# Kernel optimization log

Measured on AMD Instinct MI355X. Metric: run time of the kernel, lower is better.

## Reference

```python
import jax, jax.numpy as jnp
import numpy as np
from jax import lax

# ---- config (matches DecodePredictions init kwargs) ----
MAX_PER_CLASS = 100
MAX_TOTAL = 100
IOU_THRESH = 0.5
SCORE_THRESH = 0.05
NUM_CLASSES = 80
K_CAND = 512  # per-class candidate pool kept before NMS (bounds the O(K^2) IoU work)
BOX_VARIANCE = np.array([0.1, 0.1, 0.2, 0.2], np.float32)


def generate_anchors(height, width):
    """RetinaNet anchors (keras.io AnchorBox): FPN levels 3-7, 3 ratios x 3 scales, [cx,cy,w,h] in pixels."""
    ratios = [0.5, 1.0, 2.0]
    scales = [2 ** 0.0, 2 ** (1.0 / 3.0), 2 ** (2.0 / 3.0)]
    all_anchors = []
    for level in range(3, 8):
        stride = 2 ** level
        area = float((2 ** (level + 2)) ** 2)  # 32^2 .. 512^2
        dims = []
        for r in ratios:
            ah = np.sqrt(area / r)
            aw = area / ah
            for s in scales:
                dims.append([s * aw, s * ah])
        dims = np.asarray(dims, np.float32)  # [9, 2] = (w, h)
        fh = int(np.ceil(height / stride))
        fw = int(np.ceil(width / stride))
        rx = (np.arange(fw, dtype=np.float32) + 0.5) * stride
        ry = (np.arange(fh, dtype=np.float32) + 0.5) * stride
        cx, cy = np.meshgrid(rx, ry)
        centers = np.stack([cx, cy], -1)[:, :, None, :].repeat(9, axis=2)  # [fh,fw,9,2]
        d = np.broadcast_to(dims, (fh, fw, 9, 2))
        all_anchors.append(np.concatenate([centers, d], -1).reshape(-1, 4).astype(np.float32))
    return jnp.asarray(np.concatenate(all_anchors, 0))  # [N, 4]


def _pairwise_iou(b):
    # Generic TF NMS IoU formula treating coords as [y1,x1,y2,x2] (module feeds cx,cy,w,h -- replicated faithfully).
    y1, x1, y2, x2 = b[:, 0], b[:, 1], b[:, 2], b[:, 3]
    area = jnp.maximum(y2 - y1, 0.0) * jnp.maximum(x2 - x1, 0.0)
    ih = jnp.maximum(jnp.minimum(y2[:, None], y2[None, :]) - jnp.maximum(y1[:, None], y1[None, :]), 0.0)
    iw = jnp.maximum(jnp.minimum(x2[:, None], x2[None, :]) - jnp.maximum(x1[:, None], x1[None, :]), 0.0)
    inter = ih * iw
    union = area[:, None] + area[None, :] - inter
    return jnp.where(union > 0.0, inter / union, 0.0)


def _nms_single_class(boxes, scores):  # boxes [N,4], scores [N]
    top_s, idx = lax.top_k(scores, K_CAND)          # sort-by-score candidate pool
    top_b = boxes[idx]                               # [K,4]
    keep0 = top_s > SCORE_THRESH                     # score_threshold filter
    iou = _pairwise_iou(top_b)                       # [K,K]
    rng = jnp.arange(K_CAND)

    def body(i, keep):
        sup = (iou[i] > IOU_THRESH) & (rng > i)      # boxes ranked below i suppressed by i
        return jnp.where(keep[i], keep & ~sup, keep)

    keep = lax.fori_loop(0, K_CAND, body, keep0)
    kept_s = jnp.where(keep, top_s, 0.0)
    sel_s, sel = lax.top_k(kept_s, MAX_PER_CLASS)    # max_output_size_per_class
    return top_b[sel], sel_s                         # [P,4], [P]


def _combine(cls_boxes, cls_scores):  # [C,P,4], [C,P] -> combined top MAX_TOTAL for one image
    C, P = cls_scores.shape
    flat_s = cls_scores.reshape(-1)
    flat_b = cls_boxes.reshape(-1, 4)
    flat_c = jnp.repeat(jnp.arange(C, dtype=jnp.float32), P)
    top_s, idx = lax.top_k(flat_s, MAX_TOTAL)
    valid = (top_s > 0.0)
    vf = valid.astype(flat_b.dtype)
    boxes = jnp.clip(flat_b[idx], 0.0, 1.0) * vf[:, None]  # clip_boxes=True, zero-pad invalid
    scores = top_s * vf
    classes = jnp.where(valid, flat_c[idx], 0.0)
    return boxes, scores, classes, valid.sum().astype(jnp.int32)


def _forward(inputs, predictions):
    H, W = inputs.shape[1], inputs.shape[2]
    anchors = generate_anchors(float(H), float(W))            # [N,4] cx,cy,w,h
    cls_scores = jax.nn.sigmoid(predictions[..., :-4])        # [B,N,C]
    box_pred = predictions[..., -4:] * jnp.asarray(BOX_VARIANCE)
    xy = box_pred[..., :2] * anchors[..., 2:] + anchors[..., :2]
    wh = jnp.exp(box_pred[..., 2:]) * anchors[..., 2:]
    boxes = jnp.concatenate([xy, wh], -1)                     # [B,N,4] decoded

    per_class = jax.vmap(jax.vmap(_nms_single_class, in_axes=(None, 1)), in_axes=(0, 0))
    cb, cs = per_class(boxes, cls_scores)                     # [B,C,P,4], [B,C,P]
    return jax.vmap(_combine)(cb, cs)                         # boxes, scores, classes, valid


def setup_inputs() -> dict:
    key = jax.random.key(0)
    k1, k2 = jax.random.split(key)
    inputs = jax.random.uniform(k1, (4, 640, 640, 3), jnp.float32)
    predictions = jax.random.normal(k2, (4, 76725, NUM_CLASSES + 4), jnp.float32)
    return {"inputs": inputs, "predictions": predictions}


def reference(inputs, predictions):
    return _forward(inputs, predictions)
```

## Files before the change

kernel.cpp:

```cpp
#include <hip/hip_runtime.h>
#include <cmath>

#define NA 76725
#define NCLS 80
#define NB 4
#define KC 512
#define MPC 100
#define MT 100
#define TT 128
#define NTILE 600
#define NSLOTP 600
#define PADN 76800
#define CAP 4096
#define SLOT 16
#define SPLIT 8
#define THRESH_LOGIT 2.0f

struct Dims { float d[5 * 9 * 2]; };


__device__ __forceinline__ unsigned keyof(float x) {
    unsigned u = __float_as_uint(x);
    return u ^ ((u & 0x80000000u) ? 0xFFFFFFFFu : 0x80000000u);
}
__device__ __forceinline__ float unkey(unsigned k) {
    unsigned u = (k & 0x80000000u) ? (k ^ 0x80000000u) : ~k;
    return __uint_as_float(u);
}
__device__ __forceinline__ float sigmoidf_dev(float x) {
    if (x >= 0.f) return 1.f / (1.f + expf(-x));
    float e = expf(x);
    return e / (1.f + e);
}
__device__ __forceinline__ unsigned long long compose(unsigned key, int a) {
    return ((unsigned long long)key << 32) | (unsigned long long)(0xFFFFFFFFu - (unsigned)a);
}

__device__ __forceinline__ float4 decode_box(float4 p, int a, const Dims& dims) {
    const int base[5] = {0, 57600, 72000, 75600, 76500};
    const int fw[5] = {80, 40, 20, 10, 5};
    const float strd[5] = {8.f, 16.f, 32.f, 64.f, 128.f};
    int l;
    if (a < 57600) l = 0;
    else if (a < 72000) l = 1;
    else if (a < 75600) l = 2;
    else if (a < 76500) l = 3;
    else l = 4;
    int i = a - base[l];
    int cell = i / 9, k = i - cell * 9;
    int x = cell % fw[l], y = cell / fw[l];
    float cx = ((float)x + 0.5f) * strd[l];
    float cy = ((float)y + 0.5f) * strd[l];
    float aw = dims.d[(l * 9 + k) * 2 + 0];
    float ah = dims.d[(l * 9 + k) * 2 + 1];
    float bx = __fmul_rn(p.x, 0.1f), by = __fmul_rn(p.y, 0.1f);
    float bw = __fmul_rn(p.z, 0.2f), bh = __fmul_rn(p.w, 0.2f);
    float4 o;
    o.x = __fadd_rn(__fmul_rn(bx, aw), cx);
    o.y = __fadd_rn(__fmul_rn(by, ah), cy);
    o.z = __fmul_rn(expf(bw), aw);
    o.w = __fmul_rn(expf(bh), ah);
    return o;
}


__global__ __launch_bounds__(256) void scan_kernel(const float* __restrict__ pred,
                                                   unsigned long long* __restrict__ candbuf,
                                                   int* __restrict__ counts2) {
    __shared__ int cnt[NCLS];
    const int blk = blockIdx.x;
    const int b = blk / NTILE, tix = blk - b * NTILE;
    const int t0 = tix * TT;
    int nrow = NA - t0; if (nrow > TT) nrow = TT;

    if (threadIdx.x < NCLS) cnt[threadIdx.x] = 0;
    __syncthreads();

    const float4* src = reinterpret_cast<const float4*>(pred + ((size_t)b * NA + t0) * 84);
    const int nv = nrow * 21;
    unsigned long long* slotbase = candbuf + (size_t)(b * NCLS) * NSLOTP * SLOT + (size_t)tix * SLOT;
    for (int i = threadIdx.x; i < nv; i += 256) {
        const float4 v = src[i];
        const int row = i / 21, chunk = i - row * 21;
        if (chunk == 20) continue;
        const int a = t0 + row, cbase = chunk * 4;
        const float vals[4] = {v.x, v.y, v.z, v.w};
        #pragma unroll
        for (int q = 0; q < 4; ++q) {
            if (vals[q] > THRESH_LOGIT) {
                const int c = cbase + q;
                const int p = atomicAdd(&cnt[c], 1);
                if (p < SLOT)
                    slotbase[(size_t)c * NSLOTP * SLOT + p] = compose(keyof(vals[q]), a);
            }
        }
    }
    __syncthreads();
    if (threadIdx.x < NCLS)
        counts2[(size_t)(b * NCLS + threadIdx.x) * NSLOTP + tix] = cnt[threadIdx.x];
}


__device__ __forceinline__ void find_bin(int* hist, int bins, int remaining,
                                         int* sh3, int* wsum) {
    const int tid = threadIdx.x;
    const int lane = tid & 63, wv = tid >> 6;
    const int nit = (bins + 1023) >> 10;
    int lsum = 0;
    for (int q = 0; q < nit; ++q) {
        int rr = tid * nit + q;
        if (rr < bins) lsum += hist[bins - 1 - rr];
    }
    int acc = lsum;
    #pragma unroll
    for (int off = 1; off < 64; off <<= 1) {
        int x = __shfl_up(acc, off);
        if (lane >= off) acc += x;
    }
    if (lane == 63) wsum[wv] = acc;
    __syncthreads();
    int base = 0;
    for (int w = 0; w < wv; ++w) base += wsum[w];
    int run = base + acc - lsum;
    for (int q = 0; q < nit; ++q) {
        int rr = tid * nit + q;
        if (rr < bins) {
            int h = hist[bins - 1 - rr];
            if (run < remaining && remaining <= run + h) { sh3[0] = bins - 1 - rr; sh3[1] = run; sh3[2] = h; }
            run += h;
        }
    }
    __syncthreads();
}


__global__ __launch_bounds__(1024) void topk2_kernel(const float* __restrict__ pred,
                                                     const unsigned long long* __restrict__ candbuf,
                                                     const int* __restrict__ counts2,
                                                     float* __restrict__ top_score,
                                                     float4* __restrict__ sel_boxes, Dims dims) {
    const int col = blockIdx.x;
    const int b = col / NCLS, cc = col - b * NCLS;
    const int tid = threadIdx.x;
    const int lane = tid & 63, wv = tid >> 6;

    __shared__ unsigned long long cand[CAP];
    __shared__ int hist[256];
    __shared__ unsigned long long buf[KC];
    __shared__ int scnt[NSLOTP];
    __shared__ int spfx[NSLOTP];
    __shared__ int sh3[3];
    __shared__ int wsum[16];
    __shared__ int gcount, eqtaken, totsh, ovfsh;
    __shared__ int wcnt[16];
    int* hist4k = (int*)cand;

    if (tid == 0) { totsh = 0; ovfsh = 0; }
    if (tid < NSLOTP) scnt[tid] = counts2[(size_t)col * NSLOTP + tid];
    __syncthreads();

    int lsum = (tid < NSLOTP) ? scnt[tid] : 0;
    if (lsum > SLOT) ovfsh = 1;
    int acc = lsum;
    #pragma unroll
    for (int off = 1; off < 64; off <<= 1) {
        int x = __shfl_up(acc, off);
        if (lane >= off) acc += x;
    }
    if (lane == 63) wsum[wv] = acc;
    __syncthreads();
    int base = 0;
    for (int w = 0; w < wv; ++w) base += wsum[w];
    if (tid < NSLOTP) spfx[tid] = base + acc - lsum;
    if (tid == 1023) totsh = base + acc;
    __syncthreads();

    const int tot = totsh;
    const bool fastok = (!ovfsh) && tot >= KC && tot <= CAP;
    int nc = -1;

    if (fastok) {
        const unsigned long long* src = candbuf + (size_t)col * NSLOTP * SLOT;
        for (int i = tid; i < NSLOTP * SLOT; i += 1024) {
            const int e = i >> 4, q = i & (SLOT - 1);
            const unsigned long long v = src[i];
            if (q < scnt[e]) cand[spfx[e] + q] = v;
        }
        nc = tot;
        __syncthreads();
    } else {
        const float* colp = pred + (size_t)b * NA * 84 + cc;
        for (int i = tid; i < 4096; i += 1024) hist4k[i] = 0;
        __syncthreads();
        for (int a = tid; a < NA; a += 1024)
            atomicAdd(&hist4k[keyof(colp[(size_t)a * 84]) >> 20], 1);
        __syncthreads();
        find_bin(hist4k, 4096, KC, sh3, wsum);
        const int bsel = sh3[0], above = sh3[1], ceq1 = sh3[2];
        const int ncand = above + ceq1;

        if (ncand <= CAP) {
            const unsigned fk = ((unsigned)bsel) << 20;
            if (tid == 0) gcount = 0;
            __syncthreads();
            for (int a = tid; a < NA; a += 1024) {
                unsigned k = keyof(colp[(size_t)a * 84]);
                if (k >= fk) { int p = atomicAdd(&gcount, 1); cand[p] = compose(k, a); }
            }
            __syncthreads();
            nc = gcount;
        } else {
            unsigned prefix = ((unsigned)bsel) << 20;
            int remaining = KC - above;

            for (int i = tid; i < 4096; i += 1024) hist4k[i] = 0;
            __syncthreads();
            for (int a = tid; a < NA; a += 1024) {
                unsigned k = keyof(colp[(size_t)a * 84]);
                if ((k & 0xFFF00000u) == prefix) atomicAdd(&hist4k[(k >> 8) & 4095], 1);
            }
            __syncthreads();
            find_bin(hist4k, 4096, remaining, sh3, wsum);
            prefix |= ((unsigned)sh3[0]) << 8;
            remaining -= sh3[1];

            if (tid < 256) hist[tid] = 0;
            __syncthreads();
            for (int a = tid; a < NA; a += 1024) {
                unsigned k = keyof(colp[(size_t)a * 84]);
                if ((k & 0xFFFFFF00u) == prefix) atomicAdd(&hist[k & 255], 1);
            }
            __syncthreads();
            find_bin(hist, 256, remaining, sh3, wsum);
            prefix |= (unsigned)sh3[0];
            remaining -= sh3[1];

            const unsigned K = prefix;
            const int cgt = KC - remaining;
            const int need = remaining;
            if (tid == 0) { gcount = 0; eqtaken = 0; }
            __syncthreads();
            for (int bs = 0; bs < PADN; bs += 1024) {
                int a = bs + tid;
                unsigned key = (a < NA) ? keyof(colp[(size_t)a * 84]) : 0u;
                if (a < NA && key > K) {
                    int p = atomicAdd(&gcount, 1);
                    buf[p] = compose(key, a);
                }
                bool eq = (key == K) && (a < NA);
                unsigned long long m = __ballot(eq);
                if (lane == 0) wcnt[wv] = __popcll(m);
                __syncthreads();
                int off = eqtaken;
                for (int w = 0; w < wv; ++w) off += wcnt[w];
                int rank = off + __popcll(m & ((1ull << lane) - 1ull));
                if (eq && rank < need)
                    buf[cgt + rank] = compose(K, a);
                __syncthreads();
                if (tid == 0) {
                    int s = 0;
                    for (int w = 0; w < 16; ++w) s += wcnt[w];
                    eqtaken += s;
                }
                __syncthreads();
            }
            nc = -1;
        }
    }

    if (nc >= 0) {
        unsigned long long cpre = 0ull;
        int rem512 = KC;
        for (int pass = 0; pass < 8; ++pass) {
            const int shift = 56 - 8 * pass;
            const unsigned long long mdone = pass ? ((~0ull) << (shift + 8)) : 0ull;
            if (tid < 256) hist[tid] = 0;
            __syncthreads();
            for (int t = tid; t < nc; t += 1024) {
                unsigned long long k = cand[t];
                if ((k & mdone) == cpre) atomicAdd(&hist[(int)((k >> shift) & 255)], 1);
            }
            __syncthreads();
            find_bin(hist, 256, rem512, sh3, wsum);
            cpre |= ((unsigned long long)(unsigned)sh3[0]) << shift;
            rem512 -= sh3[1];
            __syncthreads();
        }
        if (tid == 0) gcount = 0;
        __syncthreads();
        for (int t = tid; t < nc; t += 1024) {
            unsigned long long k = cand[t];
            if (k >= cpre) { int p = atomicAdd(&gcount, 1); buf[p] = k; }
        }
        __syncthreads();
    }

    for (int k2 = 2; k2 <= KC; k2 <<= 1) {
        for (int j = k2 >> 1; j > 0; j >>= 1) {
            __syncthreads();
            if (tid < KC) {
                int i = tid, ixj = i ^ j;
                if (ixj > i) {
                    unsigned long long A = buf[i], B = buf[ixj];
                    bool up = (i & k2) == 0;
                    if (up ? (A < B) : (A > B)) { buf[i] = B; buf[ixj] = A; }
                }
            }
        }
    }
    __syncthreads();
    if (tid < KC) {
        unsigned long long v = buf[tid];
        unsigned key = (unsigned)(v >> 32);
        int a = (int)(0xFFFFFFFFu - (unsigned)(v & 0xFFFFFFFFu));
        top_score[col * KC + tid] = sigmoidf_dev(unkey(key));
        const float4 p4 = *reinterpret_cast<const float4*>(pred + ((size_t)b * NA + a) * 84 + 80);
        sel_boxes[(size_t)col * KC + tid] = decode_box(p4, a, dims);
    }
}


__global__ __launch_bounds__(512) void nms_build_kernel(const float4* __restrict__ sel_boxes,
                                                        unsigned long long* __restrict__ maskbuf) {
    const int blk = blockIdx.x;
    const int col = blk >> 3, part = blk & 7;
    const int tid = threadIdx.x, wave = tid >> 6, lane = tid & 63;
    __shared__ float y1[KC], x1[KC], y2[KC], x2[KC], ar[KC];

    for (int t = tid; t < KC; t += 512) {
        float4 bx = sel_boxes[(size_t)col * KC + t];
        y1[t] = bx.x; x1[t] = bx.y; y2[t] = bx.z; x2[t] = bx.w;
        ar[t] = __fmul_rn(fmaxf(__fsub_rn(bx.z, bx.x), 0.f),
                          fmaxf(__fsub_rn(bx.w, bx.y), 0.f));
    }
    __syncthreads();

    float jy1[8], jx1[8], jy2[8], jx2[8], jar[8];
    #pragma unroll
    for (int w = 0; w < 8; ++w) {
        int j = (w << 6) + lane;
        jy1[w] = y1[j]; jx1[w] = x1[j]; jy2[w] = y2[j]; jx2[w] = x2[j]; jar[w] = ar[j];
    }

    for (int k = 0; k < 8; ++k) {
        const int i = part + SPLIT * (wave + 8 * k);
        const float iy1 = y1[i], ix1 = x1[i], iy2 = y2[i], ix2 = x2[i], iar = ar[i];
        unsigned long long row[8];
        #pragma unroll
        for (int w = 0; w < 8; ++w) {
            unsigned long long m = 0ull;
            if (((w << 6) + 63) > i) {
                const int j = (w << 6) + lane;
                float ih = fmaxf(__fsub_rn(fminf(iy2, jy2[w]), fmaxf(iy1, jy1[w])), 0.f);
                float iw = fmaxf(__fsub_rn(fminf(ix2, jx2[w]), fmaxf(ix1, jx1[w])), 0.f);
                float inter = __fmul_rn(ih, iw);
                float uni = __fsub_rn(__fadd_rn(iar, jar[w]), inter);
                m = __ballot((uni > 0.f) && (inter > __fmul_rn(0.5f, uni)) && (j > i));
            }
            row[w] = m;
        }
        unsigned long long v = row[0];
        v = (lane == 1) ? row[1] : v;
        v = (lane == 2) ? row[2] : v;
        v = (lane == 3) ? row[3] : v;
        v = (lane == 4) ? row[4] : v;
        v = (lane == 5) ? row[5] : v;
        v = (lane == 6) ? row[6] : v;
        v = (lane == 7) ? row[7] : v;
        if (lane < 8) maskbuf[((size_t)col * KC + i) * 8 + lane] = v;
    }
}


__global__ __launch_bounds__(256) void nms_resolve_kernel(const float4* __restrict__ sel_boxes,
                                                          const float* __restrict__ top_score,
                                                          const unsigned long long* __restrict__ maskbuf,
                                                          float4* __restrict__ col_boxes,
                                                          float* __restrict__ col_scores) {
    const int col = blockIdx.x;
    const int tid = threadIdx.x, wv = tid >> 6, lane = tid & 63;
    __shared__ unsigned long long mask[KC * 8];
    __shared__ float y1[KC], x1[KC], y2[KC], x2[KC], sc[KC];
    __shared__ unsigned long long keep0w[8], keepw[8];
    __shared__ int wordpfx[9];
    __shared__ int sel[MPC];

    {
        const unsigned long long* src = maskbuf + (size_t)col * KC * 8;
        for (int m = tid; m < KC * 8; m += 256) mask[m] = src[m];
    }
    for (int t = tid; t < KC; t += 256) {
        float4 bx = sel_boxes[(size_t)col * KC + t];
        y1[t] = bx.x; x1[t] = bx.y; y2[t] = bx.z; x2[t] = bx.w;
        const float s = top_score[col * KC + t];
        sc[t] = s;
        const unsigned long long m = __ballot(s > 0.05f);
        if (lane == 0) keep0w[t >> 6] = m;
    }
    __syncthreads();

    if (wv == 0) {
        const int w8 = lane & 7;
        const unsigned long long kww = keep0w[w8];
        unsigned long long remw = 0ull;
        for (int ib = 0; ib < KC; ib += 8) {
            unsigned long long rows[8];
            #pragma unroll
            for (int u = 0; u < 8; ++u) rows[u] = mask[(ib + u) * 8 + w8];
            #pragma unroll
            for (int u = 0; u < 8; ++u) {
                const int i = ib + u, W = i >> 6, t = i & 63;
                const unsigned long long remW = __shfl(remw, W);
                const unsigned long long kwW = __shfl(kww, W);
                if (((kwW >> t) & 1ull) && !((remW >> t) & 1ull)) remw |= rows[u];
            }
        }
        if (lane < 8) keepw[w8] = kww & ~remw;
    }
    __syncthreads();
    if (tid == 0) {
        int s = 0;
        #pragma unroll
        for (int w = 0; w < 8; ++w) { wordpfx[w] = s; s += __popcll(keepw[w]); }
        wordpfx[8] = s;
    }
    __syncthreads();

    const int nkept = wordpfx[8];
    for (int t = tid; t < KC; t += 256) {
        const unsigned long long w = keepw[t >> 6];
        const int l = t & 63;
        const bool kp = (w >> l) & 1ull;
        const int kb = wordpfx[t >> 6] + __popcll(w & ((1ull << l) - 1ull));
        if (kp) {
            if (kb < MPC) sel[kb] = t;
        } else {
            const int nb = t - kb;
            if (nkept + nb < MPC) sel[nkept + nb] = t;
        }
    }
    __syncthreads();
    if (tid < MPC) {
        int t = sel[tid];
        bool kp = (keepw[t >> 6] >> (t & 63)) & 1ull;
        col_scores[col * MPC + tid] = kp ? sc[t] : 0.f;
        col_boxes[col * MPC + tid] = make_float4(y1[t], x1[t], y2[t], x2[t]);
    }
}


__global__ __launch_bounds__(1024) void combine_kernel(const float4* __restrict__ col_boxes,
                                                       const float* __restrict__ col_scores,
                                                       float* __restrict__ out) {
    const int b = blockIdx.x, tid = threadIdx.x;
    const int wv = tid >> 6, lane = tid & 63;
    __shared__ int hist[256];
    __shared__ unsigned long long cand[128];
    __shared__ int sh3[3];
    __shared__ int gcnt, eqtaken;
    __shared__ int wcnt[16];
    __shared__ int wsc[16];

    const int NTOT = NCLS * MPC;
    unsigned sck[8];
    #pragma unroll
    for (int q = 0; q < 8; ++q) {
        const int t = (q << 10) + tid;
        sck[q] = (t < NTOT) ? __float_as_uint(col_scores[b * NTOT + t]) : 0u;
    }

    unsigned prefix = 0;
    int remaining = MT, ceq = 0;
    #pragma unroll 1
    for (int pass = 0; pass < 4; ++pass) {
        const int shift = 24 - 8 * pass;
        const unsigned mdone = pass ? (0xFFFFFFFFu << (shift + 8)) : 0u;
        if (tid < 256) hist[tid] = 0;
        __syncthreads();
        #pragma unroll
        for (int q = 0; q < 8; ++q) {
            const int t = (q << 10) + tid;
            if (t < NTOT && (sck[q] & mdone) == prefix)
                atomicAdd(&hist[(sck[q] >> shift) & 255], 1);
        }
        __syncthreads();
        int lsum = (tid < 256) ? hist[255 - tid] : 0;
        int acc2 = lsum;
        #pragma unroll
        for (int off = 1; off < 64; off <<= 1) {
            int x = __shfl_up(acc2, off);
            if (lane >= off) acc2 += x;
        }
        if (lane == 63) wsc[wv] = acc2;
        __syncthreads();
        int base2 = 0;
        for (int w = 0; w < wv; ++w) base2 += wsc[w];
        int run = base2 + acc2 - lsum;
        if (tid < 256 && run < remaining && remaining <= run + lsum) { sh3[0] = 255 - tid; sh3[1] = run; sh3[2] = lsum; }
        __syncthreads();
        prefix |= ((unsigned)sh3[0]) << shift;
        remaining -= sh3[1];
        ceq = sh3[2];
        __syncthreads();
    }
    const unsigned S = prefix;
    const int cgt = MT - remaining;

    if (tid == 0) { gcnt = 0; eqtaken = 0; }
    if (tid < 128) cand[tid] = 0ull;
    __syncthreads();
    #pragma unroll
    for (int q = 0; q < 8; ++q) {
        const int t = (q << 10) + tid;
        if (t < NTOT && sck[q] > S) {
            int p = atomicAdd(&gcnt, 1);
            cand[p] = ((unsigned long long)sck[q] << 32) |
                      (unsigned long long)(0xFFFFFFFFu - (unsigned)t);
        }
    }
    __syncthreads();

    if (ceq == remaining) {
        #pragma unroll
        for (int q = 0; q < 8; ++q) {
            const int t = (q << 10) + tid;
            if (t < NTOT && sck[q] == S) {
                int p = atomicAdd(&eqtaken, 1);
                cand[cgt + p] = ((unsigned long long)S << 32) |
                                (unsigned long long)(0xFFFFFFFFu - (unsigned)t);
            }
        }
        __syncthreads();
    } else {
        #pragma unroll 1
        for (int q = 0; q < 8; ++q) {
            const int t = (q << 10) + tid;
            const bool eq = (t < NTOT) && (sck[q] == S);
            unsigned long long m = __ballot(eq);
            if (lane == 0) wcnt[wv] = __popcll(m);
            __syncthreads();
            int off = eqtaken;
            for (int w = 0; w < wv; ++w) off += wcnt[w];
            int rank = off + __popcll(m & ((1ull << lane) - 1ull));
            if (eq && rank < remaining)
                cand[cgt + rank] = ((unsigned long long)S << 32) |
                                   (unsigned long long)(0xFFFFFFFFu - (unsigned)t);
            __syncthreads();
            if (tid == 0) {
                int s = 0;
                for (int w = 0; w < 16; ++w) s += wcnt[w];
                eqtaken += s;
            }
            __syncthreads();
        }
    }

    for (int k2 = 2; k2 <= 128; k2 <<= 1) {
        for (int j = k2 >> 1; j > 0; j >>= 1) {
            __syncthreads();
            if (tid < 128) {
                int i = tid, ixj = i ^ j;
                if (ixj > i) {
                    unsigned long long A = cand[i], B = cand[ixj];
                    bool up = (i & k2) == 0;
                    if (up ? (A < B) : (A > B)) { cand[i] = B; cand[ixj] = A; }
                }
            }
        }
    }
    __syncthreads();
    if (tid == 0) gcnt = 0;
    __syncthreads();
    if (tid < MT) {
        unsigned long long v = cand[tid];
        float s = __uint_as_float((unsigned)(v >> 32));
        int f = (int)(0xFFFFFFFFu - (unsigned)(v & 0xFFFFFFFFu));
        bool valid = (s > 0.f);
        int cl = 0, p = 0;
        float4 bx = make_float4(0.f, 0.f, 0.f, 0.f);
        if (valid) {
            cl = f / MPC;
            p = f - cl * MPC;
            float4 raw = col_boxes[((size_t)b * NCLS + cl) * MPC + p];
            bx.x = fminf(fmaxf(raw.x, 0.f), 1.f);
            bx.y = fminf(fmaxf(raw.y, 0.f), 1.f);
            bx.z = fminf(fmaxf(raw.z, 0.f), 1.f);
            bx.w = fminf(fmaxf(raw.w, 0.f), 1.f);
            atomicAdd(&gcnt, 1);
        }
        int o = b * MT + tid;
        out[o * 4 + 0] = bx.x;
        out[o * 4 + 1] = bx.y;
        out[o * 4 + 2] = bx.z;
        out[o * 4 + 3] = bx.w;
        out[NB * MT * 4 + o] = valid ? s : 0.f;
        out[NB * MT * 5 + o] = valid ? (float)cl : 0.f;
    }
    __syncthreads();
    if (tid == 0) out[NB * MT * 6 + b] = (float)gcnt;
}


extern "C" void kernel_launch(void* const* d_in, const int* in_sizes, int n_in,
                              void* d_out, int out_size, void* d_ws, size_t ws_size,
                              hipStream_t stream) {
    const float* pred = (const float*)d_in[1];
    float* out = (float*)d_out;
    char* ws = (char*)d_ws;

    Dims dims;
    const double ratios[3] = {0.5, 1.0, 2.0};
    for (int l = 0; l < 5; ++l) {
        double side = (double)(1 << (l + 5));
        double area = side * side;
        for (int ri = 0; ri < 3; ++ri) {
            double ah = sqrt(area / ratios[ri]);
            double aw = area / ah;
            for (int si = 0; si < 3; ++si) {
                double s = pow(2.0, (double)si / 3.0);
                dims.d[(l * 9 + ri * 3 + si) * 2 + 0] = (float)(s * aw);
                dims.d[(l * 9 + ri * 3 + si) * 2 + 1] = (float)(s * ah);
            }
        }
    }

    const size_t SZ_CAND = (size_t)NB * NCLS * NSLOTP * SLOT * 8;
    const size_t SZ_CNT  = (size_t)NB * NCLS * NSLOTP * 4;
    const size_t SZ_SC   = (size_t)NB * NCLS * KC * 4;
    const size_t SZ_SEL  = (size_t)NB * NCLS * KC * 16;
    const size_t SZ_CB   = (size_t)NB * NCLS * MPC * 16;

    unsigned long long* candbuf    = (unsigned long long*)(ws);
    int*                counts2    = (int*)(ws + SZ_CAND);
    float*              top_score  = (float*)(ws + SZ_CAND + SZ_CNT);
    float4*             sel_boxes  = (float4*)(ws + SZ_CAND + SZ_CNT + SZ_SC);
    float4*             col_boxes  = (float4*)(ws + SZ_CAND + SZ_CNT + SZ_SC + SZ_SEL);
    float*              col_scores = (float*)(ws + SZ_CAND + SZ_CNT + SZ_SC + SZ_SEL + SZ_CB);
    unsigned long long* maskbuf    = (unsigned long long*)(ws);

    scan_kernel<<<NB * NTILE, 256, 0, stream>>>(pred, candbuf, counts2);
    topk2_kernel<<<NB * NCLS, 1024, 0, stream>>>(pred, candbuf, counts2, top_score, sel_boxes, dims);
    nms_build_kernel<<<NB * NCLS * SPLIT, 512, 0, stream>>>(sel_boxes, maskbuf);
    nms_resolve_kernel<<<NB * NCLS, 256, 0, stream>>>(sel_boxes, top_score, maskbuf, col_boxes, col_scores);
    combine_kernel<<<NB, 1024, 0, stream>>>(col_boxes, col_scores, out);
}
```

Before: 321.8 us.

## Fuse top-k selection, NMS mask build and resolve into one kernel

Merges the top-k, NMS mask-build and NMS resolve kernels into a single 512-thread per-column kernel. Boxes, scores and the suppression mask now stay in shared memory instead of going through global buffers, which removes two launches and the intermediate traffic. The scan kernel's candidate buffer changes to a tile-major layout so each tile writes contiguously, and its loop is unrolled four times to issue more loads in flight. The cost is less parallelism in mask building: 320 blocks each compute all 512 rows instead of 2560 blocks, so per-block work rises.

```diff
diff --git a/kernel.cpp b/kernel.cpp
--- a/kernel.cpp
+++ b/kernel.cpp
@@ -10,10 +10,10 @@
 #define TT 128
 #define NTILE 600
 #define NSLOTP 600
+#define NSLOTPAD 1024
 #define PADN 76800
 #define CAP 4096
 #define SLOT 16
-#define SPLIT 8
 #define THRESH_LOGIT 2.0f
 
 struct Dims { float d[5 * 9 * 2]; };
@@ -78,23 +78,39 @@
 
     const float4* src = reinterpret_cast<const float4*>(pred + ((size_t)b * NA + t0) * 84);
     const int nv = nrow * 21;
-    unsigned long long* slotbase = candbuf + (size_t)(b * NCLS) * NSLOTP * SLOT + (size_t)tix * SLOT;
-    for (int i = threadIdx.x; i < nv; i += 256) {
+    unsigned long long* slotbase = candbuf + (size_t)(b * NTILE + tix) * NCLS * SLOT;
+
+    #define PROC(v, idx) do {                                                  \
+        const int row_ = (idx) / 21, chunk_ = (idx) - row_ * 21;               \
+        if (chunk_ != 20) {                                                    \
+            const int a_ = t0 + row_, cbase_ = chunk_ * 4;                     \
+            const float vals_[4] = {(v).x, (v).y, (v).z, (v).w};               \
+            _Pragma("unroll")                                                  \
+            for (int q_ = 0; q_ < 4; ++q_) {                                   \
+                if (vals_[q_] > THRESH_LOGIT) {                                \
+                    const int c_ = cbase_ + q_;                                \
+                    const int p_ = atomicAdd(&cnt[c_], 1);                     \
+                    if (p_ < SLOT)                                             \
+                        slotbase[c_ * SLOT + p_] = compose(keyof(vals_[q_]), a_); \
+                }                                                              \
+            }                                                                  \
+        }                                                                      \
+    } while (0)
+
+    int i = threadIdx.x;
+    for (; i + 768 < nv; i += 1024) {
+        const float4 v0 = src[i];
+        const float4 v1 = src[i + 256];
+        const float4 v2 = src[i + 512];
+        const float4 v3 = src[i + 768];
+        PROC(v0, i); PROC(v1, i + 256); PROC(v2, i + 512); PROC(v3, i + 768);
+    }
+    for (; i < nv; i += 256) {
         const float4 v = src[i];
-        const int row = i / 21, chunk = i - row * 21;
-        if (chunk == 20) continue;
-        const int a = t0 + row, cbase = chunk * 4;
-        const float vals[4] = {v.x, v.y, v.z, v.w};
-        #pragma unroll
-        for (int q = 0; q < 4; ++q) {
-            if (vals[q] > THRESH_LOGIT) {
-                const int c = cbase + q;
-                const int p = atomicAdd(&cnt[c], 1);
-                if (p < SLOT)
-                    slotbase[(size_t)c * NSLOTP * SLOT + p] = compose(keyof(vals[q]), a);
-            }
-        }
-    }
+        PROC(v, i);
+    }
+    #undef PROC
+
     __syncthreads();
     if (threadIdx.x < NCLS)
         counts2[(size_t)(b * NCLS + threadIdx.x) * NSLOTP + tix] = cnt[threadIdx.x];
@@ -105,7 +121,7 @@
                                          int* sh3, int* wsum) {
     const int tid = threadIdx.x;
     const int lane = tid & 63, wv = tid >> 6;
-    const int nit = (bins + 1023) >> 10;
+    const int nit = (bins + 511) >> 9;
     int lsum = 0;
     for (int q = 0; q < nit; ++q) {
         int rr = tid * nit + q;
@@ -134,11 +150,11 @@
 }
 
 
-__global__ __launch_bounds__(1024) void topk2_kernel(const float* __restrict__ pred,
+__global__ __launch_bounds__(512) void topnms_kernel(const float* __restrict__ pred,
                                                      const unsigned long long* __restrict__ candbuf,
                                                      const int* __restrict__ counts2,
-                                                     float* __restrict__ top_score,
-                                                     float4* __restrict__ sel_boxes, Dims dims) {
+                                                     float4* __restrict__ col_boxes,
+                                                     float* __restrict__ col_scores, Dims dims) {
     const int col = blockIdx.x;
     const int b = col / NCLS, cc = col - b * NCLS;
     const int tid = threadIdx.x;
@@ -147,21 +163,28 @@
     __shared__ unsigned long long cand[CAP];
     __shared__ int hist[256];
     __shared__ unsigned long long buf[KC];
-    __shared__ int scnt[NSLOTP];
-    __shared__ int spfx[NSLOTP];
+    __shared__ int scnt[NSLOTPAD];
+    __shared__ int spfx[NSLOTPAD];
+    __shared__ float y1[KC], x1[KC], y2[KC], x2[KC], ar[KC], sc[KC];
+    __shared__ unsigned long long keep0w[8], keepw[8];
+    __shared__ int wordpfx[9];
+    __shared__ int sel[MPC];
     __shared__ int sh3[3];
-    __shared__ int wsum[16];
+    __shared__ int wsum[8];
     __shared__ int gcount, eqtaken, totsh, ovfsh;
-    __shared__ int wcnt[16];
+    __shared__ int wcnt[8];
     int* hist4k = (int*)cand;
+    unsigned long long* maskl = cand;
 
     if (tid == 0) { totsh = 0; ovfsh = 0; }
-    if (tid < NSLOTP) scnt[tid] = counts2[(size_t)col * NSLOTP + tid];
-    __syncthreads();
-
-    int lsum = (tid < NSLOTP) ? scnt[tid] : 0;
-    if (lsum > SLOT) ovfsh = 1;
-    int acc = lsum;
+    for (int i = tid; i < NSLOTPAD; i += 512)
+        scnt[i] = (i < NSLOTP) ? counts2[(size_t)col * NSLOTP + i] : 0;
+    __syncthreads();
+
+    const int c0s = scnt[2 * tid], c1s = scnt[2 * tid + 1];
+    if (c0s > SLOT || c1s > SLOT) ovfsh = 1;
+    const int pair = c0s + c1s;
+    int acc = pair;
     #pragma unroll
     for (int off = 1; off < 64; off <<= 1) {
         int x = __shfl_up(acc, off);
@@ -171,8 +194,10 @@
     __syncthreads();
     int base = 0;
     for (int w = 0; w < wv; ++w) base += wsum[w];
-    if (tid < NSLOTP) spfx[tid] = base + acc - lsum;
-    if (tid == 1023) totsh = base + acc;
+    const int excl = base + acc - pair;
+    spfx[2 * tid] = excl;
+    spfx[2 * tid + 1] = excl + c0s;
+    if (tid == 511) totsh = base + acc;
     __syncthreads();
 
     const int tot = totsh;
@@ -180,19 +205,19 @@
     int nc = -1;
 
     if (fastok) {
-        const unsigned long long* src = candbuf + (size_t)col * NSLOTP * SLOT;
-        for (int i = tid; i < NSLOTP * SLOT; i += 1024) {
+        const size_t colbase = (size_t)(b * NTILE) * (NCLS * SLOT) + (size_t)cc * SLOT;
+        for (int i = tid; i < NSLOTP * SLOT; i += 512) {
             const int e = i >> 4, q = i & (SLOT - 1);
-            const unsigned long long v = src[i];
+            const unsigned long long v = candbuf[colbase + (size_t)e * (NCLS * SLOT) + q];
             if (q < scnt[e]) cand[spfx[e] + q] = v;
         }
         nc = tot;
         __syncthreads();
     } else {
         const float* colp = pred + (size_t)b * NA * 84 + cc;
-        for (int i = tid; i < 4096; i += 1024) hist4k[i] = 0;
-        __syncthreads();
-        for (int a = tid; a < NA; a += 1024)
+        for (int i = tid; i < 4096; i += 512) hist4k[i] = 0;
+        __syncthreads();
+        for (int a = tid; a < NA; a += 512)
             atomicAdd(&hist4k[keyof(colp[(size_t)a * 84]) >> 20], 1);
         __syncthreads();
         find_bin(hist4k, 4096, KC, sh3, wsum);
@@ -203,7 +228,7 @@
             const unsigned fk = ((unsigned)bsel) << 20;
             if (tid == 0) gcount = 0;
             __syncthreads();
-            for (int a = tid; a < NA; a += 1024) {
+            for (int a = tid; a < NA; a += 512) {
                 unsigned k = keyof(colp[(size_t)a * 84]);
                 if (k >= fk) { int p = atomicAdd(&gcount, 1); cand[p] = compose(k, a); }
             }
@@ -213,9 +238,9 @@
             unsigned prefix = ((unsigned)bsel) << 20;
             int remaining = KC - above;
 
-            for (int i = tid; i < 4096; i += 1024) hist4k[i] = 0;
-            __syncthreads();
-            for (int a = tid; a < NA; a += 1024) {
+            for (int i = tid; i < 4096; i += 512) hist4k[i] = 0;
+            __syncthreads();
+            for (int a = tid; a < NA; a += 512) {
                 unsigned k = keyof(colp[(size_t)a * 84]);
                 if ((k & 0xFFF00000u) == prefix) atomicAdd(&hist4k[(k >> 8) & 4095], 1);
             }
@@ -226,7 +251,7 @@
 
             if (tid < 256) hist[tid] = 0;
             __syncthreads();
-            for (int a = tid; a < NA; a += 1024) {
+            for (int a = tid; a < NA; a += 512) {
                 unsigned k = keyof(colp[(size_t)a * 84]);
                 if ((k & 0xFFFFFF00u) == prefix) atomicAdd(&hist[k & 255], 1);
             }
@@ -240,7 +265,7 @@
             const int need = remaining;
             if (tid == 0) { gcount = 0; eqtaken = 0; }
             __syncthreads();
-            for (int bs = 0; bs < PADN; bs += 1024) {
+            for (int bs = 0; bs < PADN; bs += 512) {
                 int a = bs + tid;
                 unsigned key = (a < NA) ? keyof(colp[(size_t)a * 84]) : 0u;
                 if (a < NA && key > K) {
@@ -259,7 +284,7 @@
                 __syncthreads();
                 if (tid == 0) {
                     int s = 0;
-                    for (int w = 0; w < 16; ++w) s += wcnt[w];
+                    for (int w = 0; w < 8; ++w) s += wcnt[w];
                     eqtaken += s;
                 }
                 __syncthreads();
@@ -276,7 +301,7 @@
             const unsigned long long mdone = pass ? ((~0ull) << (shift + 8)) : 0ull;
             if (tid < 256) hist[tid] = 0;
             __syncthreads();
-            for (int t = tid; t < nc; t += 1024) {
+            for (int t = tid; t < nc; t += 512) {
                 unsigned long long k = cand[t];
                 if ((k & mdone) == cpre) atomicAdd(&hist[(int)((k >> shift) & 255)], 1);
             }
@@ -288,7 +313,7 @@
         }
         if (tid == 0) gcount = 0;
         __syncthreads();
-        for (int t = tid; t < nc; t += 1024) {
+        for (int t = tid; t < nc; t += 512) {
             unsigned long long k = cand[t];
             if (k >= cpre) { int p = atomicAdd(&gcount, 1); buf[p] = k; }
         }
@@ -298,7 +323,7 @@
     for (int k2 = 2; k2 <= KC; k2 <<= 1) {
         for (int j = k2 >> 1; j > 0; j >>= 1) {
             __syncthreads();
-            if (tid < KC) {
+            {
                 int i = tid, ixj = i ^ j;
                 if (ixj > i) {
                     unsigned long long A = buf[i], B = buf[ixj];
@@ -309,93 +334,57 @@
         }
     }
     __syncthreads();
-    if (tid < KC) {
-        unsigned long long v = buf[tid];
-        unsigned key = (unsigned)(v >> 32);
-        int a = (int)(0xFFFFFFFFu - (unsigned)(v & 0xFFFFFFFFu));
-        top_score[col * KC + tid] = sigmoidf_dev(unkey(key));
+
+    {
+        const unsigned long long v = buf[tid];
+        const unsigned key = (unsigned)(v >> 32);
+        const int a = (int)(0xFFFFFFFFu - (unsigned)(v & 0xFFFFFFFFu));
+        const float s = sigmoidf_dev(unkey(key));
+        sc[tid] = s;
         const float4 p4 = *reinterpret_cast<const float4*>(pred + ((size_t)b * NA + a) * 84 + 80);
-        sel_boxes[(size_t)col * KC + tid] = decode_box(p4, a, dims);
-    }
-}
-
-
-__global__ __launch_bounds__(512) void nms_build_kernel(const float4* __restrict__ sel_boxes,
-                                                        unsigned long long* __restrict__ maskbuf) {
-    const int blk = blockIdx.x;
-    const int col = blk >> 3, part = blk & 7;
-    const int tid = threadIdx.x, wave = tid >> 6, lane = tid & 63;
-    __shared__ float y1[KC], x1[KC], y2[KC], x2[KC], ar[KC];
-
-    for (int t = tid; t < KC; t += 512) {
-        float4 bx = sel_boxes[(size_t)col * KC + t];
-        y1[t] = bx.x; x1[t] = bx.y; y2[t] = bx.z; x2[t] = bx.w;
-        ar[t] = __fmul_rn(fmaxf(__fsub_rn(bx.z, bx.x), 0.f),
-                          fmaxf(__fsub_rn(bx.w, bx.y), 0.f));
-    }
-    __syncthreads();
-
-    float jy1[8], jx1[8], jy2[8], jx2[8], jar[8];
-    #pragma unroll
-    for (int w = 0; w < 8; ++w) {
-        int j = (w << 6) + lane;
-        jy1[w] = y1[j]; jx1[w] = x1[j]; jy2[w] = y2[j]; jx2[w] = x2[j]; jar[w] = ar[j];
-    }
-
-    for (int k = 0; k < 8; ++k) {
-        const int i = part + SPLIT * (wave + 8 * k);
-        const float iy1 = y1[i], ix1 = x1[i], iy2 = y2[i], ix2 = x2[i], iar = ar[i];
-        unsigned long long row[8];
+        const float4 bx = decode_box(p4, a, dims);
+        y1[tid] = bx.x; x1[tid] = bx.y; y2[tid] = bx.z; x2[tid] = bx.w;
+        ar[tid] = __fmul_rn(fmaxf(__fsub_rn(bx.z, bx.x), 0.f),
+                            fmaxf(__fsub_rn(bx.w, bx.y), 0.f));
+        const unsigned long long m = __ballot(s > 0.05f);
+        if (lane == 0) keep0w[tid >> 6] = m;
+    }
+    __syncthreads();
+
+    {
+        float jy1[8], jx1[8], jy2[8], jx2[8], jar[8];
         #pragma unroll
         for (int w = 0; w < 8; ++w) {
-            unsigned long long m = 0ull;
-            if (((w << 6) + 63) > i) {
-                const int j = (w << 6) + lane;
-                float ih = fmaxf(__fsub_rn(fminf(iy2, jy2[w]), fmaxf(iy1, jy1[w])), 0.f);
-                float iw = fmaxf(__fsub_rn(fminf(ix2, jx2[w]), fmaxf(ix1, jx1[w])), 0.f);
-                float inter = __fmul_rn(ih, iw);
-                float uni = __fsub_rn(__fadd_rn(iar, jar[w]), inter);
-                m = __ballot((uni > 0.f) && (inter > __fmul_rn(0.5f, uni)) && (j > i));
-            }
-            row[w] = m;
-        }
-        unsigned long long v = row[0];
-        v = (lane == 1) ? row[1] : v;
-        v = (lane == 2) ? row[2] : v;
-        v = (lane == 3) ? row[3] : v;
-        v = (lane == 4) ? row[4] : v;
-        v = (lane == 5) ? row[5] : v;
-        v = (lane == 6) ? row[6] : v;
-        v = (lane == 7) ? row[7] : v;
-        if (lane < 8) maskbuf[((size_t)col * KC + i) * 8 + lane] = v;
-    }
-}
-
-
-__global__ __launch_bounds__(256) void nms_resolve_kernel(const float4* __restrict__ sel_boxes,
-                                                          const float* __restrict__ top_score,
-                                                          const unsigned long long* __restrict__ maskbuf,
-                                                          float4* __restrict__ col_boxes,
-                                                          float* __restrict__ col_scores) {
-    const int col = blockIdx.x;
-    const int tid = threadIdx.x, wv = tid >> 6, lane = tid & 63;
-    __shared__ unsigned long long mask[KC * 8];
-    __shared__ float y1[KC], x1[KC], y2[KC], x2[KC], sc[KC];
-    __shared__ unsigned long long keep0w[8], keepw[8];
-    __shared__ int wordpfx[9];
-    __shared__ int sel[MPC];
-
-    {
-        const unsigned long long* src = maskbuf + (size_t)col * KC * 8;
-        for (int m = tid; m < KC * 8; m += 256) mask[m] = src[m];
-    }
-    for (int t = tid; t < KC; t += 256) {
-        float4 bx = sel_boxes[(size_t)col * KC + t];
-        y1[t] = bx.x; x1[t] = bx.y; y2[t] = bx.z; x2[t] = bx.w;
-        const float s = top_score[col * KC + t];
-        sc[t] = s;
-        const unsigned long long m = __ballot(s > 0.05f);
-        if (lane == 0) keep0w[t >> 6] = m;
+            int j = (w << 6) + lane;
+            jy1[w] = y1[j]; jx1[w] = x1[j]; jy2[w] = y2[j]; jx2[w] = x2[j]; jar[w] = ar[j];
+        }
+        for (int k = 0; k < 64; ++k) {
+            const int i = wv + 8 * k;
+            const float iy1 = y1[i], ix1 = x1[i], iy2 = y2[i], ix2 = x2[i], iar = ar[i];
+            unsigned long long row[8];
+            #pragma unroll
+            for (int w = 0; w < 8; ++w) {
+                unsigned long long m = 0ull;
+                if (((w << 6) + 63) > i) {
+                    const int j = (w << 6) + lane;
+                    float ih = fmaxf(__fsub_rn(fminf(iy2, jy2[w]), fmaxf(iy1, jy1[w])), 0.f);
+                    float iw = fmaxf(__fsub_rn(fminf(ix2, jx2[w]), fmaxf(ix1, jx1[w])), 0.f);
+                    float inter = __fmul_rn(ih, iw);
+                    float uni = __fsub_rn(__fadd_rn(iar, jar[w]), inter);
+                    m = __ballot((uni > 0.f) && (inter > __fmul_rn(0.5f, uni)) && (j > i));
+                }
+                row[w] = m;
+            }
+            unsigned long long v = row[0];
+            v = (lane == 1) ? row[1] : v;
+            v = (lane == 2) ? row[2] : v;
+            v = (lane == 3) ? row[3] : v;
+            v = (lane == 4) ? row[4] : v;
+            v = (lane == 5) ? row[5] : v;
+            v = (lane == 6) ? row[6] : v;
+            v = (lane == 7) ? row[7] : v;
+            if (lane < 8) maskl[i * 8 + lane] = v;
+        }
     }
     __syncthreads();
 
@@ -406,7 +395,7 @@
         for (int ib = 0; ib < KC; ib += 8) {
             unsigned long long rows[8];
             #pragma unroll
-            for (int u = 0; u < 8; ++u) rows[u] = mask[(ib + u) * 8 + w8];
+            for (int u = 0; u < 8; ++u) rows[u] = maskl[(ib + u) * 8 + w8];
             #pragma unroll
             for (int u = 0; u < 8; ++u) {
                 const int i = ib + u, W = i >> 6, t = i & 63;
@@ -427,7 +416,8 @@
     __syncthreads();
 
     const int nkept = wordpfx[8];
-    for (int t = tid; t < KC; t += 256) {
+    {
+        const int t = tid;
         const unsigned long long w = keepw[t >> 6];
         const int l = t & 63;
         const bool kp = (w >> l) & 1ull;
@@ -626,21 +616,14 @@
 
     const size_t SZ_CAND = (size_t)NB * NCLS * NSLOTP * SLOT * 8;
     const size_t SZ_CNT  = (size_t)NB * NCLS * NSLOTP * 4;
-    const size_t SZ_SC   = (size_t)NB * NCLS * KC * 4;
-    const size_t SZ_SEL  = (size_t)NB * NCLS * KC * 16;
     const size_t SZ_CB   = (size_t)NB * NCLS * MPC * 16;
 
     unsigned long long* candbuf    = (unsigned long long*)(ws);
     int*                counts2    = (int*)(ws + SZ_CAND);
-    float*              top_score  = (float*)(ws + SZ_CAND + SZ_CNT);
-    float4*             sel_boxes  = (float4*)(ws + SZ_CAND + SZ_CNT + SZ_SC);
-    float4*             col_boxes  = (float4*)(ws + SZ_CAND + SZ_CNT + SZ_SC + SZ_SEL);
-    float*              col_scores = (float*)(ws + SZ_CAND + SZ_CNT + SZ_SC + SZ_SEL + SZ_CB);
-    unsigned long long* maskbuf    = (unsigned long long*)(ws);
+    float4*             col_boxes  = (float4*)(ws + SZ_CAND + SZ_CNT);
+    float*              col_scores = (float*)(ws + SZ_CAND + SZ_CNT + SZ_CB);
 
     scan_kernel<<<NB * NTILE, 256, 0, stream>>>(pred, candbuf, counts2);
-    topk2_kernel<<<NB * NCLS, 1024, 0, stream>>>(pred, candbuf, counts2, top_score, sel_boxes, dims);
-    nms_build_kernel<<<NB * NCLS * SPLIT, 512, 0, stream>>>(sel_boxes, maskbuf);
-    nms_resolve_kernel<<<NB * NCLS, 256, 0, stream>>>(sel_boxes, top_score, maskbuf, col_boxes, col_scores);
+    topnms_kernel<<<NB * NCLS, 512, 0, stream>>>(pred, candbuf, counts2, col_boxes, col_scores, dims);
     combine_kernel<<<NB, 1024, 0, stream>>>(col_boxes, col_scores, out);
 }
```

Result: slower. 339.5 us (+5.5%).

## Replace radix top-k select with full bitonic sort of up to 1024 candidates

Applied to the files above, without the earlier changes.

The candidate threshold logit rises so fewer candidates are kept, the candidate cap drops from 4096 to 1024, and the scan tile doubles to 256 rows, halving the slot count. The 8-pass radix select over the candidate pool is replaced by a zero-padded 1024-element bitonic sort in shared memory. The top-k kernel now runs with 512 threads and packs the histogram, candidate and prefix arrays into one overlapping shared buffer. The higher threshold makes the fast path depend on at least 512 logits per class exceeding 2.3, so more classes may drop to the slow full-column path.

```diff
diff --git a/kernel.cpp b/kernel.cpp
--- a/kernel.cpp
+++ b/kernel.cpp
@@ -7,14 +7,14 @@
 #define KC 512
 #define MPC 100
 #define MT 100
-#define TT 128
-#define NTILE 600
-#define NSLOTP 600
+#define TT 256
+#define NTILE 300
+#define NSLOTP 300
 #define PADN 76800
-#define CAP 4096
+#define NCAND 1024
 #define SLOT 16
 #define SPLIT 8
-#define THRESH_LOGIT 2.0f
+#define THRESH_LOGIT 2.3f
 
 struct Dims { float d[5 * 9 * 2]; };
 
@@ -78,7 +78,7 @@
 
     const float4* src = reinterpret_cast<const float4*>(pred + ((size_t)b * NA + t0) * 84);
     const int nv = nrow * 21;
-    unsigned long long* slotbase = candbuf + (size_t)(b * NCLS) * NSLOTP * SLOT + (size_t)tix * SLOT;
+    unsigned long long* slotbase = candbuf + ((size_t)(b * NCLS) * NSLOTP + tix) * SLOT;
     for (int i = threadIdx.x; i < nv; i += 256) {
         const float4 v = src[i];
         const int row = i / 21, chunk = i - row * 21;
@@ -105,7 +105,7 @@
                                          int* sh3, int* wsum) {
     const int tid = threadIdx.x;
     const int lane = tid & 63, wv = tid >> 6;
-    const int nit = (bins + 1023) >> 10;
+    const int nit = (bins + 511) >> 9;
     int lsum = 0;
     for (int q = 0; q < nit; ++q) {
         int rr = tid * nit + q;
@@ -134,32 +134,30 @@
 }
 
 
-__global__ __launch_bounds__(1024) void topk2_kernel(const float* __restrict__ pred,
-                                                     const unsigned long long* __restrict__ candbuf,
-                                                     const int* __restrict__ counts2,
-                                                     float* __restrict__ top_score,
-                                                     float4* __restrict__ sel_boxes, Dims dims) {
+__global__ __launch_bounds__(512) void topk2_kernel(const float* __restrict__ pred,
+                                                    const unsigned long long* __restrict__ candbuf,
+                                                    const int* __restrict__ counts2,
+                                                    float* __restrict__ top_score,
+                                                    float4* __restrict__ sel_boxes, Dims dims) {
     const int col = blockIdx.x;
     const int b = col / NCLS, cc = col - b * NCLS;
     const int tid = threadIdx.x;
     const int lane = tid & 63, wv = tid >> 6;
 
-    __shared__ unsigned long long cand[CAP];
+    __shared__ int hist4k[4096];
+    __shared__ unsigned long long buf[KC];
     __shared__ int hist[256];
-    __shared__ unsigned long long buf[KC];
-    __shared__ int scnt[NSLOTP];
-    __shared__ int spfx[NSLOTP];
     __shared__ int sh3[3];
-    __shared__ int wsum[16];
+    __shared__ int wsum[8];
     __shared__ int gcount, eqtaken, totsh, ovfsh;
-    __shared__ int wcnt[16];
-    int* hist4k = (int*)cand;
+    __shared__ int wcnt[8];
+    unsigned long long* cand = (unsigned long long*)hist4k;
+    int* scnt = hist4k + 2048;
+    int* spfx = hist4k + 2560;
 
     if (tid == 0) { totsh = 0; ovfsh = 0; }
-    if (tid < NSLOTP) scnt[tid] = counts2[(size_t)col * NSLOTP + tid];
-    __syncthreads();
-
-    int lsum = (tid < NSLOTP) ? scnt[tid] : 0;
+    int lsum = (tid < NSLOTP) ? counts2[(size_t)col * NSLOTP + tid] : 0;
+    scnt[tid] = lsum;
     if (lsum > SLOT) ovfsh = 1;
     int acc = lsum;
     #pragma unroll
@@ -171,51 +169,53 @@
     __syncthreads();
     int base = 0;
     for (int w = 0; w < wv; ++w) base += wsum[w];
-    if (tid < NSLOTP) spfx[tid] = base + acc - lsum;
-    if (tid == 1023) totsh = base + acc;
+    spfx[tid] = base + acc - lsum;
+    if (tid == 511) totsh = base + acc;
     __syncthreads();
 
     const int tot = totsh;
-    const bool fastok = (!ovfsh) && tot >= KC && tot <= CAP;
-    int nc = -1;
+    const bool fastok = (!ovfsh) && tot >= KC && tot <= NCAND;
+    int mode = 0;
 
     if (fastok) {
+        cand[tid] = 0ull; cand[tid + 512] = 0ull;
+        __syncthreads();
         const unsigned long long* src = candbuf + (size_t)col * NSLOTP * SLOT;
-        for (int i = tid; i < NSLOTP * SLOT; i += 1024) {
+        for (int i = tid; i < NSLOTP * SLOT; i += 512) {
             const int e = i >> 4, q = i & (SLOT - 1);
             const unsigned long long v = src[i];
             if (q < scnt[e]) cand[spfx[e] + q] = v;
         }
-        nc = tot;
         __syncthreads();
     } else {
         const float* colp = pred + (size_t)b * NA * 84 + cc;
-        for (int i = tid; i < 4096; i += 1024) hist4k[i] = 0;
-        __syncthreads();
-        for (int a = tid; a < NA; a += 1024)
+        for (int i = tid; i < 4096; i += 512) hist4k[i] = 0;
+        __syncthreads();
+        for (int a = tid; a < NA; a += 512)
             atomicAdd(&hist4k[keyof(colp[(size_t)a * 84]) >> 20], 1);
         __syncthreads();
         find_bin(hist4k, 4096, KC, sh3, wsum);
         const int bsel = sh3[0], above = sh3[1], ceq1 = sh3[2];
         const int ncand = above + ceq1;
 
-        if (ncand <= CAP) {
+        if (ncand <= NCAND) {
             const unsigned fk = ((unsigned)bsel) << 20;
             if (tid == 0) gcount = 0;
-            __syncthreads();
-            for (int a = tid; a < NA; a += 1024) {
+            cand[tid] = 0ull; cand[tid + 512] = 0ull;
+            __syncthreads();
+            for (int a = tid; a < NA; a += 512) {
                 unsigned k = keyof(colp[(size_t)a * 84]);
                 if (k >= fk) { int p = atomicAdd(&gcount, 1); cand[p] = compose(k, a); }
             }
             __syncthreads();
-            nc = gcount;
         } else {
+            mode = 1;
             unsigned prefix = ((unsigned)bsel) << 20;
             int remaining = KC - above;
 
-            for (int i = tid; i < 4096; i += 1024) hist4k[i] = 0;
-            __syncthreads();
-            for (int a = tid; a < NA; a += 1024) {
+            for (int i = tid; i < 4096; i += 512) hist4k[i] = 0;
+            __syncthreads();
+            for (int a = tid; a < NA; a += 512) {
                 unsigned k = keyof(colp[(size_t)a * 84]);
                 if ((k & 0xFFF00000u) == prefix) atomicAdd(&hist4k[(k >> 8) & 4095], 1);
             }
@@ -226,7 +226,7 @@
 
             if (tid < 256) hist[tid] = 0;
             __syncthreads();
-            for (int a = tid; a < NA; a += 1024) {
+            for (int a = tid; a < NA; a += 512) {
                 unsigned k = keyof(colp[(size_t)a * 84]);
                 if ((k & 0xFFFFFF00u) == prefix) atomicAdd(&hist[k & 255], 1);
             }
@@ -240,7 +240,7 @@
             const int need = remaining;
             if (tid == 0) { gcount = 0; eqtaken = 0; }
             __syncthreads();
-            for (int bs = 0; bs < PADN; bs += 1024) {
+            for (int bs = 0; bs < PADN; bs += 512) {
                 int a = bs + tid;
                 unsigned key = (a < NA) ? keyof(colp[(size_t)a * 84]) : 0u;
                 if (a < NA && key > K) {
@@ -259,60 +259,49 @@
                 __syncthreads();
                 if (tid == 0) {
                     int s = 0;
-                    for (int w = 0; w < 16; ++w) s += wcnt[w];
+                    for (int w = 0; w < 8; ++w) s += wcnt[w];
                     eqtaken += s;
                 }
                 __syncthreads();
             }
-            nc = -1;
-        }
-    }
-
-    if (nc >= 0) {
-        unsigned long long cpre = 0ull;
-        int rem512 = KC;
-        for (int pass = 0; pass < 8; ++pass) {
-            const int shift = 56 - 8 * pass;
-            const unsigned long long mdone = pass ? ((~0ull) << (shift + 8)) : 0ull;
-            if (tid < 256) hist[tid] = 0;
-            __syncthreads();
-            for (int t = tid; t < nc; t += 1024) {
-                unsigned long long k = cand[t];
-                if ((k & mdone) == cpre) atomicAdd(&hist[(int)((k >> shift) & 255)], 1);
-            }
-            __syncthreads();
-            find_bin(hist, 256, rem512, sh3, wsum);
-            cpre |= ((unsigned long long)(unsigned)sh3[0]) << shift;
-            rem512 -= sh3[1];
-            __syncthreads();
-        }
-        if (tid == 0) gcount = 0;
-        __syncthreads();
-        for (int t = tid; t < nc; t += 1024) {
-            unsigned long long k = cand[t];
-            if (k >= cpre) { int p = atomicAdd(&gcount, 1); buf[p] = k; }
-        }
-        __syncthreads();
-    }
-
-    for (int k2 = 2; k2 <= KC; k2 <<= 1) {
-        for (int j = k2 >> 1; j > 0; j >>= 1) {
-            __syncthreads();
-            if (tid < KC) {
-                int i = tid, ixj = i ^ j;
-                if (ixj > i) {
-                    unsigned long long A = buf[i], B = buf[ixj];
-                    bool up = (i & k2) == 0;
-                    if (up ? (A < B) : (A > B)) { buf[i] = B; buf[ixj] = A; }
+        }
+    }
+
+    if (mode == 0) {
+        for (int k2 = 2; k2 <= NCAND; k2 <<= 1) {
+            for (int j = k2 >> 1; j > 0; j >>= 1) {
+                __syncthreads();
+                for (int i = tid; i < NCAND; i += 512) {
+                    int ixj = i ^ j;
+                    if (ixj > i) {
+                        unsigned long long A = cand[i], B = cand[ixj];
+                        bool up = (i & k2) == 0;
+                        if (up ? (A < B) : (A > B)) { cand[i] = B; cand[ixj] = A; }
+                    }
                 }
             }
         }
-    }
-    __syncthreads();
-    if (tid < KC) {
-        unsigned long long v = buf[tid];
-        unsigned key = (unsigned)(v >> 32);
-        int a = (int)(0xFFFFFFFFu - (unsigned)(v & 0xFFFFFFFFu));
+    } else {
+        for (int k2 = 2; k2 <= KC; k2 <<= 1) {
+            for (int j = k2 >> 1; j > 0; j >>= 1) {
+                __syncthreads();
+                {
+                    int i = tid, ixj = i ^ j;
+                    if (ixj > i) {
+                        unsigned long long A = buf[i], B = buf[ixj];
+                        bool up = (i & k2) == 0;
+                        if (up ? (A < B) : (A > B)) { buf[i] = B; buf[ixj] = A; }
+                    }
+                }
+            }
+        }
+    }
+    __syncthreads();
+
+    {
+        const unsigned long long v = (mode == 0) ? cand[tid] : buf[tid];
+        const unsigned key = (unsigned)(v >> 32);
+        const int a = (int)(0xFFFFFFFFu - (unsigned)(v & 0xFFFFFFFFu));
         top_score[col * KC + tid] = sigmoidf_dev(unkey(key));
         const float4 p4 = *reinterpret_cast<const float4*>(pred + ((size_t)b * NA + a) * 84 + 80);
         sel_boxes[(size_t)col * KC + tid] = decode_box(p4, a, dims);
@@ -639,7 +628,7 @@
     unsigned long long* maskbuf    = (unsigned long long*)(ws);
 
     scan_kernel<<<NB * NTILE, 256, 0, stream>>>(pred, candbuf, counts2);
-    topk2_kernel<<<NB * NCLS, 1024, 0, stream>>>(pred, candbuf, counts2, top_score, sel_boxes, dims);
+    topk2_kernel<<<NB * NCLS, 512, 0, stream>>>(pred, candbuf, counts2, top_score, sel_boxes, dims);
     nms_build_kernel<<<NB * NCLS * SPLIT, 512, 0, stream>>>(sel_boxes, maskbuf);
     nms_resolve_kernel<<<NB * NCLS, 256, 0, stream>>>(sel_boxes, top_score, maskbuf, col_boxes, col_scores);
     combine_kernel<<<NB, 1024, 0, stream>>>(col_boxes, col_scores, out);
```

Result: faster. 304.6 us (-5.3%).
